# Performance work log

Measured on AMD Instinct MI355X. Metric: run time of the kernel, lower is better.

## Reference

```python
import jax, jax.numpy as jnp
import numpy as np

N = 100000       # nodes
E = 1600000      # edges (before self-loops)
IN = 32          # input_dim
HID = 64         # hidden_dim
HEADS = 4
HO = HID // HEADS  # per-head out of gat1
OUT = 32         # output_dim
HID2 = HID // 2
BN_EPS = 1e-5
NEG_SLOPE = 0.2  # PyG GATConv default leaky relu slope


def setup_inputs() -> dict:
    key = jax.random.key(0)
    ks = jax.random.split(key, 28)
    f32 = jnp.float32
    rn = lambda k, s, sc=0.1: jax.random.normal(k, s, f32) * sc
    inp = {}
    inp["x"] = jax.random.normal(ks[0], (N, IN), f32)
    inp["edge_index"] = jax.random.randint(ks[1], (2, E), 0, N, jnp.int32)
    # GATConv 1: in=IN, heads=HEADS, out/head=HO, concat
    inp["W1"] = rn(ks[2], (IN, HEADS * HO))
    inp["att_src1"] = rn(ks[3], (HEADS, HO))
    inp["att_dst1"] = rn(ks[4], (HEADS, HO))
    inp["b1"] = rn(ks[5], (HEADS * HO,))
    # GATConv 2: in=HID, heads=1, out=OUT, no concat (mean)
    inp["W2"] = rn(ks[6], (HID, OUT))
    inp["att_src2"] = rn(ks[7], (1, OUT))
    inp["att_dst2"] = rn(ks[8], (1, OUT))
    inp["b2"] = rn(ks[9], (OUT,))
    # BatchNorms (inference mode: running stats)
    inp["bn1_g"] = jnp.ones((HID,), f32)
    inp["bn1_b"] = jnp.zeros((HID,), f32)
    inp["bn1_m"] = rn(ks[10], (HID,), 0.1)
    inp["bn1_v"] = jax.random.uniform(ks[11], (HID,), f32, 0.5, 1.5)
    inp["bn2_g"] = jnp.ones((OUT,), f32)
    inp["bn2_b"] = jnp.zeros((OUT,), f32)
    inp["bn2_m"] = rn(ks[12], (OUT,), 0.1)
    inp["bn2_v"] = jax.random.uniform(ks[13], (OUT,), f32, 0.5, 1.5)
    # classifier: OUT -> HID2 -> 3
    inp["cls_w1"] = rn(ks[14], (OUT, HID2))
    inp["cls_b1"] = rn(ks[15], (HID2,))
    inp["cls_w2"] = rn(ks[16], (HID2, 3))
    inp["cls_b2"] = rn(ks[17], (3,))
    inp["reg_w1"] = rn(ks[18], (OUT, HID2))
    inp["reg_b1"] = rn(ks[19], (HID2,))
    inp["reg_w2"] = rn(ks[20], (HID2, 1))
    inp["reg_b2"] = rn(ks[21], (1,))
    return inp


def _segment_softmax(e, seg, n):
    # e: [E, H]; softmax over edges sharing the same destination segment
    m = jax.ops.segment_max(e, seg, num_segments=n)
    ex = jnp.exp(e - m[seg])
    s = jax.ops.segment_sum(ex, seg, num_segments=n)
    return ex / (s[seg] + 1e-16)


def _gat(x, src, dst, W, a_src, a_dst, b, heads, ho, concat):
    n = x.shape[0]
    h = (x @ W).reshape(n, heads, ho)                    # [N,H,F]
    e = (h * a_src).sum(-1)[src] + (h * a_dst).sum(-1)[dst]  # [E,H]
    e = jax.nn.leaky_relu(e, NEG_SLOPE)
    alpha = _segment_softmax(e, dst, n)                  # [E,H]
    out = jax.ops.segment_sum(h[src] * alpha[:, :, None], dst, num_segments=n)
    out = out.reshape(n, heads * ho) if concat else out.mean(axis=1)
    return out + b


def _bn(x, g, b, m, v):
    return (x - m) * jax.lax.rsqrt(v + BN_EPS) * g + b


def reference(x, edge_index, W1, att_src1, att_dst1, b1, W2, att_src2, att_dst2, b2,
              bn1_g, bn1_b, bn1_m, bn1_v, bn2_g, bn2_b, bn2_m, bn2_v,
              cls_w1, cls_b1, cls_w2, cls_b2, reg_w1, reg_b1, reg_w2, reg_b2):
    n = x.shape[0]
    # PyG GATConv default add_self_loops=True
    loops = jnp.arange(n, dtype=edge_index.dtype)
    src = jnp.concatenate([edge_index[0], loops])
    dst = jnp.concatenate([edge_index[1], loops])

    h = _gat(x, src, dst, W1, att_src1, att_dst1, b1, HEADS, HO, True)   # [N, HID]
    h = jax.nn.relu(_bn(h, bn1_g, bn1_b, bn1_m, bn1_v))
    emb = _gat(h, src, dst, W2, att_src2, att_dst2, b2, 1, OUT, False)   # [N, OUT]
    emb = jax.nn.relu(_bn(emb, bn2_g, bn2_b, bn2_m, bn2_v))

    roles = jax.nn.relu(emb @ cls_w1 + cls_b1) @ cls_w2 + cls_b2          # [N, 3]
    energy = jax.nn.relu(emb @ reg_w1 + reg_b1) @ reg_w2 + reg_b2         # [N, 1]
    return emb, roles, energy
```

## Files before the change

kernel.cpp:

```cpp
#include <hip/hip_runtime.h>
#include <hip/hip_bf16.h>

#define NN 100000
#define EE 1600000
#define ETOT (EE + NN)
#define IND 32
#define HIDD 64
#define NHEADS 4
#define OUTD 32
#define HID2D 32

#define BSH 9
#define NBUCK 196
#define CAP 10240
#define EPB 2048

typedef unsigned int uint;

__device__ __forceinline__ uint pack2(float a, float b) {
  uint lo = (uint)__bfloat16_as_ushort(__float2bfloat16(a));
  uint hi = (uint)__bfloat16_as_ushort(__float2bfloat16(b));
  return (hi << 16) | lo;
}
__device__ __forceinline__ float lo2f(uint w) { return __uint_as_float(w << 16); }
__device__ __forceinline__ float hi2f(uint w) { return __uint_as_float(w & 0xFFFF0000u); }

__global__ __launch_bounds__(256) void k_lin1(
    const float* __restrict__ x, const float* __restrict__ W1,
    const float* __restrict__ atsrc, const float* __restrict__ atdst,
    uint* __restrict__ h1u, float* __restrict__ as1, float* __restrict__ ad1) {
  __shared__ float Ws[IND * HIDD];
  __shared__ float xs[8 * IND];
  __shared__ float atS[HIDD], atD[HIDD];
  int t = threadIdx.x;
  for (int i = t; i < IND * HIDD; i += 256) Ws[i] = W1[i];
  if (t < HIDD) { atS[t] = atsrc[t]; atD[t] = atdst[t]; }
  xs[t] = x[blockIdx.x * 256 + t];
  __syncthreads();
  int nl = t >> 5, tl = t & 31;
  int node = blockIdx.x * 8 + nl;
  int j0 = 2 * tl, j1 = j0 + 1;
  float a0 = 0.f, a1 = 0.f;
#pragma unroll
  for (int k = 0; k < IND; k++) {
    float xv = xs[nl * IND + k];
    a0 += xv * Ws[k * HIDD + j0];
    a1 += xv * Ws[k * HIDD + j1];
  }
  h1u[node * 32 + tl] = pack2(a0, a1);
  float ps = a0 * atS[j0] + a1 * atS[j1];
  float pd = a0 * atD[j0] + a1 * atD[j1];
#pragma unroll
  for (int off = 4; off >= 1; off >>= 1) {
    ps += __shfl_down(ps, off, 8);
    pd += __shfl_down(pd, off, 8);
  }
  if ((tl & 7) == 0) {
    as1[node * NHEADS + (tl >> 3)] = ps;
    ad1[node * NHEADS + (tl >> 3)] = pd;
  }
}

__global__ __launch_bounds__(256) void k_lin2(
    const float* __restrict__ hbn, const float* __restrict__ W2,
    const float* __restrict__ atsrc, const float* __restrict__ atdst,
    uint* __restrict__ h2u, float* __restrict__ as2, float* __restrict__ ad2) {
  __shared__ float Ws[HIDD * OUTD];
  __shared__ float xs[16 * HIDD];
  __shared__ float atS[OUTD], atD[OUTD];
  int t = threadIdx.x;
  for (int i = t; i < HIDD * OUTD; i += 256) Ws[i] = W2[i];
  if (t < OUTD) { atS[t] = atsrc[t]; atD[t] = atdst[t]; }
  for (int i = t; i < 16 * HIDD; i += 256) xs[i] = hbn[blockIdx.x * 16 * HIDD + i];
  __syncthreads();
  int nl = t >> 4, tl = t & 15;
  int node = blockIdx.x * 16 + nl;
  int j0 = 2 * tl, j1 = j0 + 1;
  float a0 = 0.f, a1 = 0.f;
#pragma unroll
  for (int k = 0; k < HIDD; k++) {
    float xv = xs[nl * HIDD + k];
    a0 += xv * Ws[k * OUTD + j0];
    a1 += xv * Ws[k * OUTD + j1];
  }
  h2u[node * 16 + tl] = pack2(a0, a1);
  float ps = a0 * atS[j0] + a1 * atS[j1];
  float pd = a0 * atD[j0] + a1 * atD[j1];
#pragma unroll
  for (int off = 8; off >= 1; off >>= 1) {
    ps += __shfl_down(ps, off, 16);
    pd += __shfl_down(pd, off, 16);
  }
  if (tl == 0) { as2[node] = ps; ad2[node] = pd; }
}

__global__ __launch_bounds__(256) void k_bin(const int* __restrict__ ei,
                                             int* __restrict__ bcur,
                                             int* __restrict__ bins) {
  __shared__ int cnt[NBUCK];
  int t = threadIdx.x;
  for (int i = t; i < NBUCK; i += 256) cnt[i] = 0;
  __syncthreads();
  int base = blockIdx.x * EPB;
  int recs[8], bks[8];
#pragma unroll
  for (int k = 0; k < 8; k++) {
    int i = base + k * 256 + t;
    recs[k] = -1; bks[k] = 0;
    if (i < ETOT) {
      int s, d;
      if (i < EE) { s = ei[i]; d = ei[EE + i]; } else { s = i - EE; d = s; }
      recs[k] = (s << BSH) | (d & ((1 << BSH) - 1));
      bks[k] = d >> BSH;
      atomicAdd(&cnt[bks[k]], 1);
    }
  }
  __syncthreads();
  for (int i = t; i < NBUCK; i += 256) cnt[i] = atomicAdd(&bcur[i], cnt[i]);
  __syncthreads();
#pragma unroll
  for (int k = 0; k < 8; k++) {
    if (recs[k] >= 0) {
      int pos = atomicAdd(&cnt[bks[k]], 1);
      bins[bks[k] * CAP + pos] = recs[k];
    }
  }
}

__global__ __launch_bounds__(256) void k_scanb(const int* __restrict__ bcur,
                                               int* __restrict__ gbase,
                                               int* __restrict__ rowp) {
  __shared__ int sA[256], sB[256];
  int t = threadIdx.x;
  int v = (t < NBUCK) ? bcur[t] : 0;
  sA[t] = v;
  __syncthreads();
  int* in = sA; int* out = sB;
  for (int off = 1; off < 256; off <<= 1) {
    out[t] = in[t] + ((t >= off) ? in[t - off] : 0);
    __syncthreads();
    int* tmp = in; in = out; out = tmp;
  }
  if (t < NBUCK) gbase[t] = in[t] - v;
  if (t == 0) rowp[NN] = ETOT;
}

__global__ __launch_bounds__(256) void k_csr(const int* __restrict__ bcur,
                                             const int* __restrict__ gbase,
                                             const int* __restrict__ bins,
                                             int* __restrict__ rowp,
                                             int* __restrict__ srcs) {
  __shared__ int lrec[CAP];
  __shared__ int ldeg[512], sA[512], sB[512];
  int b = blockIdx.x, t = threadIdx.x;
  int count = bcur[b]; if (count > CAP) count = CAP;
  int gb = gbase[b];
  for (int i = t; i < 512; i += 256) ldeg[i] = 0;
  __syncthreads();
  for (int i = t; i < count; i += 256) {
    int r = bins[b * CAP + i];
    lrec[i] = r;
    atomicAdd(&ldeg[r & 511], 1);
  }
  __syncthreads();
  for (int i = t; i < 512; i += 256) sA[i] = ldeg[i];
  __syncthreads();
  int* in = sA; int* out = sB;
  for (int off = 1; off < 512; off <<= 1) {
    for (int i = t; i < 512; i += 256)
      out[i] = in[i] + ((i >= off) ? in[i - off] : 0);
    __syncthreads();
    int* tmp = in; in = out; out = tmp;
  }
  int nb = b << BSH;
  for (int i = t; i < 512; i += 256) {
    int ex = in[i] - ldeg[i];
    if (nb + i < NN) rowp[nb + i] = gb + ex;
    ldeg[i] = ex;
  }
  __syncthreads();
  for (int i = t; i < count; i += 256) {
    int r = lrec[i];
    int pos = atomicAdd(&ldeg[r & 511], 1);
    srcs[gb + pos] = r >> BSH;
  }
}

__global__ __launch_bounds__(256) void k_agg1(
    const int* __restrict__ rowp, const int* __restrict__ srcs,
    const uint* __restrict__ h1u, const float* __restrict__ as1,
    const float* __restrict__ ad1, const float* __restrict__ b1,
    const float* __restrict__ g, const float* __restrict__ bb,
    const float* __restrict__ m, const float* __restrict__ v,
    float* __restrict__ hbn) {
  int t = threadIdx.x;
  int wid = t >> 6, lane = t & 63;
  int node = blockIdx.x * 4 + wid;
  int slot = lane >> 3;
  int fl = lane & 7;
  int hd = fl >> 1;
  int start = rowp[node], end = rowp[node + 1];
  int lastp = end - 1;
  float adv = ad1[node * NHEADS + hd];
  const uint4* h14 = (const uint4*)h1u;
  float acc[8] = {0.f, 0.f, 0.f, 0.f, 0.f, 0.f, 0.f, 0.f};
  float l = 0.f;
  int p = start + slot;
  int pc = p < lastp ? p : lastp;
  int s0 = srcs[pc];
  uint4 w = h14[s0 * 8 + fl];
  float as = as1[s0 * NHEADS + hd];
  int p1 = p + 8;
  int pc1 = p1 < lastp ? p1 : lastp;
  int s1 = srcs[pc1];
  while (p < end) {
    uint4 wn = h14[s1 * 8 + fl];
    float asn = as1[s1 * NHEADS + hd];
    int p2 = p1 + 8;
    int pc2 = p2 < lastp ? p2 : lastp;
    int s2 = srcs[pc2];
    float e = as + adv;
    e = fmaxf(e, 0.2f * e);
    float ex = __expf(e);
    l += ex;
    acc[0] += ex * lo2f(w.x); acc[1] += ex * hi2f(w.x);
    acc[2] += ex * lo2f(w.y); acc[3] += ex * hi2f(w.y);
    acc[4] += ex * lo2f(w.z); acc[5] += ex * hi2f(w.z);
    acc[6] += ex * lo2f(w.w); acc[7] += ex * hi2f(w.w);
    w = wn; as = asn; s1 = s2; p = p1; p1 = p2;
  }
#pragma unroll
  for (int off = 8; off <= 32; off <<= 1) {
#pragma unroll
    for (int i = 0; i < 8; i++) acc[i] += __shfl_xor(acc[i], off, 64);
    l += __shfl_xor(l, off, 64);
  }
  if (slot == 0) {
    float li = 1.f / (l + 1e-16f);
    int fb = fl * 8;
    float o[8];
#pragma unroll
    for (int i = 0; i < 8; i++) {
      int j = fb + i;
      float ov = acc[i] * li + b1[j];
      ov = (ov - m[j]) * rsqrtf(v[j] + 1e-5f) * g[j] + bb[j];
      o[i] = fmaxf(ov, 0.f);
    }
    float4* dst = (float4*)(hbn + node * HIDD + fb);
    dst[0] = make_float4(o[0], o[1], o[2], o[3]);
    dst[1] = make_float4(o[4], o[5], o[6], o[7]);
  }
}

__global__ __launch_bounds__(256) void k_agg2(
    const int* __restrict__ rowp, const int* __restrict__ srcs,
    const uint* __restrict__ h2u, const float* __restrict__ as2,
    const float* __restrict__ ad2, const float* __restrict__ b2v,
    const float* __restrict__ g, const float* __restrict__ bb,
    const float* __restrict__ m, const float* __restrict__ v,
    float* __restrict__ out_emb) {
  int t = threadIdx.x;
  int wid = t >> 6, lane = t & 63;
  int node = blockIdx.x * 4 + wid;
  int slot = lane >> 3;
  int fl = lane & 7;
  int start = rowp[node], end = rowp[node + 1];
  int lastp = end - 1;
  float adv = ad2[node];
  const uint2* h22 = (const uint2*)h2u;
  float acc[4] = {0.f, 0.f, 0.f, 0.f};
  float l = 0.f;
  int p = start + slot;
  int pc = p < lastp ? p : lastp;
  int s0 = srcs[pc];
  uint2 w = h22[s0 * 8 + fl];
  float as = as2[s0];
  int p1 = p + 8;
  int pc1 = p1 < lastp ? p1 : lastp;
  int s1 = srcs[pc1];
  while (p < end) {
    uint2 wn = h22[s1 * 8 + fl];
    float asn = as2[s1];
    int p2 = p1 + 8;
    int pc2 = p2 < lastp ? p2 : lastp;
    int s2 = srcs[pc2];
    float e = as + adv;
    e = fmaxf(e, 0.2f * e);
    float ex = __expf(e);
    l += ex;
    acc[0] += ex * lo2f(w.x); acc[1] += ex * hi2f(w.x);
    acc[2] += ex * lo2f(w.y); acc[3] += ex * hi2f(w.y);
    w = wn; as = asn; s1 = s2; p = p1; p1 = p2;
  }
#pragma unroll
  for (int off = 8; off <= 32; off <<= 1) {
#pragma unroll
    for (int i = 0; i < 4; i++) acc[i] += __shfl_xor(acc[i], off, 64);
    l += __shfl_xor(l, off, 64);
  }
  if (slot == 0) {
    float li = 1.f / (l + 1e-16f);
    int fb = fl * 4;
    float o[4];
#pragma unroll
    for (int i = 0; i < 4; i++) {
      int j = fb + i;
      float ov = acc[i] * li + b2v[j];
      ov = (ov - m[j]) * rsqrtf(v[j] + 1e-5f) * g[j] + bb[j];
      o[i] = fmaxf(ov, 0.f);
    }
    *(float4*)(out_emb + node * OUTD + fb) = make_float4(o[0], o[1], o[2], o[3]);
  }
}

__global__ __launch_bounds__(256) void k_mlp(
    const float* __restrict__ embf,
    const float* __restrict__ cw1, const float* __restrict__ cb1,
    const float* __restrict__ cw2, const float* __restrict__ cb2,
    const float* __restrict__ rw1, const float* __restrict__ rb1,
    const float* __restrict__ rw2, const float* __restrict__ rb2,
    float* __restrict__ out_roles, float* __restrict__ out_energy) {
  __shared__ float C1[OUTD * HID2D], R1[OUTD * HID2D];
  __shared__ float C2[HID2D * 3], CB1[HID2D], RB1[HID2D], R2[HID2D];
  __shared__ float CB2v[3], RB2v;
  int t = threadIdx.x;
  for (int i = t; i < OUTD * HID2D; i += 256) { C1[i] = cw1[i]; R1[i] = rw1[i]; }
  if (t < HID2D) { CB1[t] = cb1[t]; RB1[t] = rb1[t]; R2[t] = rw2[t]; }
  if (t < HID2D * 3) C2[t] = cw2[t];
  if (t < 3) CB2v[t] = cb2[t];
  if (t == 0) RB2v = rb2[0];
  __syncthreads();
  int node = blockIdx.x * 256 + t;
  if (node >= NN) return;
  float e[OUTD];
#pragma unroll
  for (int k = 0; k < OUTD; k++) e[k] = embf[node * OUTD + k];
  float r0 = CB2v[0], r1 = CB2v[1], r2 = CB2v[2], en = RB2v;
  for (int j = 0; j < HID2D; j++) {
    float hc = CB1[j], hr = RB1[j];
#pragma unroll
    for (int k = 0; k < OUTD; k++) {
      hc += e[k] * C1[k * HID2D + j];
      hr += e[k] * R1[k * HID2D + j];
    }
    hc = fmaxf(hc, 0.f);
    hr = fmaxf(hr, 0.f);
    r0 += hc * C2[j * 3 + 0];
    r1 += hc * C2[j * 3 + 1];
    r2 += hc * C2[j * 3 + 2];
    en += hr * R2[j];
  }
  out_roles[node * 3 + 0] = r0;
  out_roles[node * 3 + 1] = r1;
  out_roles[node * 3 + 2] = r2;
  out_energy[node] = en;
}

extern "C" void kernel_launch(void* const* d_in, const int* in_sizes, int n_in,
                              void* d_out, int out_size, void* d_ws, size_t ws_size,
                              hipStream_t stream) {
  const float* x    = (const float*)d_in[0];
  const int*   ei   = (const int*)d_in[1];
  const float* W1   = (const float*)d_in[2];
  const float* as1w = (const float*)d_in[3];
  const float* ad1w = (const float*)d_in[4];
  const float* b1   = (const float*)d_in[5];
  const float* W2   = (const float*)d_in[6];
  const float* as2w = (const float*)d_in[7];
  const float* ad2w = (const float*)d_in[8];
  const float* b2v  = (const float*)d_in[9];
  const float* bn1g = (const float*)d_in[10];
  const float* bn1b = (const float*)d_in[11];
  const float* bn1m = (const float*)d_in[12];
  const float* bn1v = (const float*)d_in[13];
  const float* bn2g = (const float*)d_in[14];
  const float* bn2b = (const float*)d_in[15];
  const float* bn2m = (const float*)d_in[16];
  const float* bn2v = (const float*)d_in[17];
  const float* cw1  = (const float*)d_in[18];
  const float* cb1  = (const float*)d_in[19];
  const float* cw2  = (const float*)d_in[20];
  const float* cb2  = (const float*)d_in[21];
  const float* rw1  = (const float*)d_in[22];
  const float* rb1  = (const float*)d_in[23];
  const float* rw2  = (const float*)d_in[24];
  const float* rb2  = (const float*)d_in[25];

  uint*  h1u = (uint*)d_ws;
  float* hbn = (float*)(h1u + NN * 32);
  float* as1 = hbn + NN * HIDD;
  float* ad1 = as1 + NN * NHEADS;
  int* rowp  = (int*)(ad1 + NN * NHEADS);
  int* srcs  = rowp + NN + 1;
  int* bcur  = srcs + ETOT;
  int* gbase = bcur + 256;
  int* bins  = (int*)hbn;
  uint* h2u  = h1u;
  float* as2 = as1;
  float* ad2 = ad1;

  float* out        = (float*)d_out;
  float* out_emb    = out;
  float* out_roles  = out + NN * OUTD;
  float* out_energy = out + NN * (OUTD + 3);

  hipMemsetAsync(bcur, 0, NBUCK * sizeof(int), stream);
  k_bin<<<(ETOT + EPB - 1) / EPB, 256, 0, stream>>>(ei, bcur, bins);
  k_scanb<<<1, 256, 0, stream>>>(bcur, gbase, rowp);
  k_csr<<<NBUCK, 256, 0, stream>>>(bcur, gbase, bins, rowp, srcs);
  k_lin1<<<NN / 8, 256, 0, stream>>>(x, W1, as1w, ad1w, h1u, as1, ad1);
  k_agg1<<<NN / 4, 256, 0, stream>>>(rowp, srcs, h1u, as1, ad1, b1, bn1g, bn1b, bn1m, bn1v, hbn);
  k_lin2<<<NN / 16, 256, 0, stream>>>(hbn, W2, as2w, ad2w, h2u, as2, ad2);
  k_agg2<<<NN / 4, 256, 0, stream>>>(rowp, srcs, h2u, as2, ad2, b2v, bn2g, bn2b, bn2m, bn2v, out_emb);
  k_mlp<<<(NN + 255) / 256, 256, 0, stream>>>(out_emb, cw1, cb1, cw2, cb2, rw1, rb1, rw2, rb2, out_roles, out_energy);
}
```

Baseline: 359.9 us.

## Fuse lin2 into agg1, MLP heads into agg2, and bucket scan into CSR

Three kernels are folded into their neighbours. The second linear layer and its attention projections now run inside the layer-1 aggregation, using a per-wave row held in shared memory. The classifier and regressor heads now run inside the layer-2 aggregation. The single-block bucket scan is recomputed redundantly in every CSR block. This removes the full-size hbn intermediate and its global round trip, the re-read of the embedding, and three launches. In exchange, every 4-node block reloads the W2 and MLP weights into shared memory, and extra block-wide syncs are added.

Result: slower. 377.3 us (+4.8%).

```diff
diff --git a/kernel.cpp b/kernel.cpp
--- a/kernel.cpp
+++ b/kernel.cpp
@@ -61,39 +61,6 @@
   }
 }
 
-__global__ __launch_bounds__(256) void k_lin2(
-    const float* __restrict__ hbn, const float* __restrict__ W2,
-    const float* __restrict__ atsrc, const float* __restrict__ atdst,
-    uint* __restrict__ h2u, float* __restrict__ as2, float* __restrict__ ad2) {
-  __shared__ float Ws[HIDD * OUTD];
-  __shared__ float xs[16 * HIDD];
-  __shared__ float atS[OUTD], atD[OUTD];
-  int t = threadIdx.x;
-  for (int i = t; i < HIDD * OUTD; i += 256) Ws[i] = W2[i];
-  if (t < OUTD) { atS[t] = atsrc[t]; atD[t] = atdst[t]; }
-  for (int i = t; i < 16 * HIDD; i += 256) xs[i] = hbn[blockIdx.x * 16 * HIDD + i];
-  __syncthreads();
-  int nl = t >> 4, tl = t & 15;
-  int node = blockIdx.x * 16 + nl;
-  int j0 = 2 * tl, j1 = j0 + 1;
-  float a0 = 0.f, a1 = 0.f;
-#pragma unroll
-  for (int k = 0; k < HIDD; k++) {
-    float xv = xs[nl * HIDD + k];
-    a0 += xv * Ws[k * OUTD + j0];
-    a1 += xv * Ws[k * OUTD + j1];
-  }
-  h2u[node * 16 + tl] = pack2(a0, a1);
-  float ps = a0 * atS[j0] + a1 * atS[j1];
-  float pd = a0 * atD[j0] + a1 * atD[j1];
-#pragma unroll
-  for (int off = 8; off >= 1; off >>= 1) {
-    ps += __shfl_down(ps, off, 16);
-    pd += __shfl_down(pd, off, 16);
-  }
-  if (tl == 0) { as2[node] = ps; ad2[node] = pd; }
-}
-
 __global__ __launch_bounds__(256) void k_bin(const int* __restrict__ ei,
                                              int* __restrict__ bcur,
                                              int* __restrict__ bins) {
@@ -127,34 +94,30 @@
   }
 }
 
-__global__ __launch_bounds__(256) void k_scanb(const int* __restrict__ bcur,
-                                               int* __restrict__ gbase,
-                                               int* __restrict__ rowp) {
-  __shared__ int sA[256], sB[256];
-  int t = threadIdx.x;
-  int v = (t < NBUCK) ? bcur[t] : 0;
-  sA[t] = v;
-  __syncthreads();
-  int* in = sA; int* out = sB;
-  for (int off = 1; off < 256; off <<= 1) {
-    out[t] = in[t] + ((t >= off) ? in[t - off] : 0);
-    __syncthreads();
-    int* tmp = in; in = out; out = tmp;
-  }
-  if (t < NBUCK) gbase[t] = in[t] - v;
-  if (t == 0) rowp[NN] = ETOT;
-}
-
 __global__ __launch_bounds__(256) void k_csr(const int* __restrict__ bcur,
-                                             const int* __restrict__ gbase,
                                              const int* __restrict__ bins,
                                              int* __restrict__ rowp,
                                              int* __restrict__ srcs) {
   __shared__ int lrec[CAP];
   __shared__ int ldeg[512], sA[512], sB[512];
   int b = blockIdx.x, t = threadIdx.x;
+  {
+    int v = (t < NBUCK) ? bcur[t] : 0;
+    sA[t] = v;
+    if (t >= 256) sA[t] = 0;
+  }
+  __syncthreads();
+  int* in = sA; int* out = sB;
+  for (int off = 1; off < 256; off <<= 1) {
+    out[t] = in[t] + ((t >= off && t < 256) ? in[t - off] : 0);
+    if (t >= 256) out[t] = 0;
+    __syncthreads();
+    int* tmp = in; in = out; out = tmp;
+  }
+  int gb = (b == 0) ? 0 : in[b - 1];
+  if (b == 0 && t == 0) rowp[NN] = ETOT;
+  __syncthreads();
   int count = bcur[b]; if (count > CAP) count = CAP;
-  int gb = gbase[b];
   for (int i = t; i < 512; i += 256) ldeg[i] = 0;
   __syncthreads();
   for (int i = t; i < count; i += 256) {
@@ -165,7 +128,7 @@
   __syncthreads();
   for (int i = t; i < 512; i += 256) sA[i] = ldeg[i];
   __syncthreads();
-  int* in = sA; int* out = sB;
+  in = sA; out = sB;
   for (int off = 1; off < 512; off <<= 1) {
     for (int i = t; i < 512; i += 256)
       out[i] = in[i] + ((i >= off) ? in[i - off] : 0);
@@ -186,14 +149,22 @@
   }
 }
 
-__global__ __launch_bounds__(256) void k_agg1(
+__global__ __launch_bounds__(256) void k_agg1f(
     const int* __restrict__ rowp, const int* __restrict__ srcs,
     const uint* __restrict__ h1u, const float* __restrict__ as1,
     const float* __restrict__ ad1, const float* __restrict__ b1,
     const float* __restrict__ g, const float* __restrict__ bb,
     const float* __restrict__ m, const float* __restrict__ v,
-    float* __restrict__ hbn) {
+    const float* __restrict__ W2, const float* __restrict__ atsrc2,
+    const float* __restrict__ atdst2,
+    uint* __restrict__ h2u, float* __restrict__ as2, float* __restrict__ ad2) {
+  __shared__ float W2s[HIDD * OUTD];
+  __shared__ float atS2s[OUTD], atD2s[OUTD];
+  __shared__ float rowS[4][HIDD];
   int t = threadIdx.x;
+  for (int i = t; i < HIDD * OUTD; i += 256) W2s[i] = W2[i];
+  if (t < OUTD) { atS2s[t] = atsrc2[t]; atD2s[t] = atdst2[t]; }
+  __syncthreads();
   int wid = t >> 6, lane = t & 63;
   int node = blockIdx.x * 4 + wid;
   int slot = lane >> 3;
@@ -238,28 +209,57 @@
   if (slot == 0) {
     float li = 1.f / (l + 1e-16f);
     int fb = fl * 8;
-    float o[8];
 #pragma unroll
     for (int i = 0; i < 8; i++) {
       int j = fb + i;
       float ov = acc[i] * li + b1[j];
       ov = (ov - m[j]) * rsqrtf(v[j] + 1e-5f) * g[j] + bb[j];
-      o[i] = fmaxf(ov, 0.f);
+      rowS[wid][j] = fmaxf(ov, 0.f);
     }
-    float4* dst = (float4*)(hbn + node * HIDD + fb);
-    dst[0] = make_float4(o[0], o[1], o[2], o[3]);
-    dst[1] = make_float4(o[4], o[5], o[6], o[7]);
-  }
-}
-
-__global__ __launch_bounds__(256) void k_agg2(
+  }
+  __syncthreads();
+  int j = lane & 31, half = lane >> 5;
+  float hv = 0.f;
+#pragma unroll
+  for (int k2 = 0; k2 < 32; k2++) {
+    int k = half * 32 + k2;
+    hv += rowS[wid][k] * W2s[k * OUTD + j];
+  }
+  hv += __shfl_xor(hv, 32, 64);
+  float ps = hv * atS2s[j], pd = hv * atD2s[j];
+#pragma unroll
+  for (int off = 1; off <= 16; off <<= 1) {
+    ps += __shfl_xor(ps, off, 64);
+    pd += __shfl_xor(pd, off, 64);
+  }
+  if (lane == 0) { as2[node] = ps; ad2[node] = pd; }
+  float hn = __shfl_down(hv, 1, 64);
+  if (half == 0 && (j & 1) == 0) h2u[node * 16 + (j >> 1)] = pack2(hv, hn);
+}
+
+__global__ __launch_bounds__(256) void k_agg2f(
     const int* __restrict__ rowp, const int* __restrict__ srcs,
     const uint* __restrict__ h2u, const float* __restrict__ as2,
     const float* __restrict__ ad2, const float* __restrict__ b2v,
     const float* __restrict__ g, const float* __restrict__ bb,
     const float* __restrict__ m, const float* __restrict__ v,
-    float* __restrict__ out_emb) {
+    const float* __restrict__ cw1, const float* __restrict__ cb1,
+    const float* __restrict__ cw2, const float* __restrict__ cb2,
+    const float* __restrict__ rw1, const float* __restrict__ rb1,
+    const float* __restrict__ rw2, const float* __restrict__ rb2,
+    float* __restrict__ out_emb, float* __restrict__ out_roles,
+    float* __restrict__ out_energy) {
+  __shared__ float C1s[OUTD * HID2D], R1s[OUTD * HID2D];
+  __shared__ float C2s[HID2D * 3], R2s[HID2D], CB1s[HID2D], RB1s[HID2D];
+  __shared__ float cb2s[3], rb2s[1];
+  __shared__ float rowE[4][OUTD];
   int t = threadIdx.x;
+  for (int i = t; i < OUTD * HID2D; i += 256) { C1s[i] = cw1[i]; R1s[i] = rw1[i]; }
+  if (t < HID2D) { CB1s[t] = cb1[t]; RB1s[t] = rb1[t]; R2s[t] = rw2[t]; }
+  if (t < HID2D * 3) C2s[t] = cw2[t];
+  if (t < 3) cb2s[t] = cb2[t];
+  if (t == 0) rb2s[0] = rb2[0];
+  __syncthreads();
   int wid = t >> 6, lane = t & 63;
   int node = blockIdx.x * 4 + wid;
   int slot = lane >> 3;
@@ -308,52 +308,38 @@
       float ov = acc[i] * li + b2v[j];
       ov = (ov - m[j]) * rsqrtf(v[j] + 1e-5f) * g[j] + bb[j];
       o[i] = fmaxf(ov, 0.f);
+      rowE[wid][j] = o[i];
     }
     *(float4*)(out_emb + node * OUTD + fb) = make_float4(o[0], o[1], o[2], o[3]);
   }
-}
-
-__global__ __launch_bounds__(256) void k_mlp(
-    const float* __restrict__ embf,
-    const float* __restrict__ cw1, const float* __restrict__ cb1,
-    const float* __restrict__ cw2, const float* __restrict__ cb2,
-    const float* __restrict__ rw1, const float* __restrict__ rb1,
-    const float* __restrict__ rw2, const float* __restrict__ rb2,
-    float* __restrict__ out_roles, float* __restrict__ out_energy) {
-  __shared__ float C1[OUTD * HID2D], R1[OUTD * HID2D];
-  __shared__ float C2[HID2D * 3], CB1[HID2D], RB1[HID2D], R2[HID2D];
-  __shared__ float CB2v[3], RB2v;
-  int t = threadIdx.x;
-  for (int i = t; i < OUTD * HID2D; i += 256) { C1[i] = cw1[i]; R1[i] = rw1[i]; }
-  if (t < HID2D) { CB1[t] = cb1[t]; RB1[t] = rb1[t]; R2[t] = rw2[t]; }
-  if (t < HID2D * 3) C2[t] = cw2[t];
-  if (t < 3) CB2v[t] = cb2[t];
-  if (t == 0) RB2v = rb2[0];
-  __syncthreads();
-  int node = blockIdx.x * 256 + t;
-  if (node >= NN) return;
-  float e[OUTD];
-#pragma unroll
-  for (int k = 0; k < OUTD; k++) e[k] = embf[node * OUTD + k];
-  float r0 = CB2v[0], r1 = CB2v[1], r2 = CB2v[2], en = RB2v;
-  for (int j = 0; j < HID2D; j++) {
-    float hc = CB1[j], hr = RB1[j];
-#pragma unroll
-    for (int k = 0; k < OUTD; k++) {
-      hc += e[k] * C1[k * HID2D + j];
-      hr += e[k] * R1[k * HID2D + j];
-    }
-    hc = fmaxf(hc, 0.f);
-    hr = fmaxf(hr, 0.f);
-    r0 += hc * C2[j * 3 + 0];
-    r1 += hc * C2[j * 3 + 1];
-    r2 += hc * C2[j * 3 + 2];
-    en += hr * R2[j];
-  }
-  out_roles[node * 3 + 0] = r0;
-  out_roles[node * 3 + 1] = r1;
-  out_roles[node * 3 + 2] = r2;
-  out_energy[node] = en;
+  __syncthreads();
+  int j = lane & 31, half = lane >> 5;
+  float a2 = half ? RB1s[j] : CB1s[j];
+  const float* Wm = half ? R1s : C1s;
+#pragma unroll
+  for (int k = 0; k < OUTD; k++) a2 += rowE[wid][k] * Wm[k * HID2D + j];
+  a2 = fmaxf(a2, 0.f);
+  float p0, p1v, p2v;
+  if (half == 0) {
+    p0 = a2 * C2s[j * 3 + 0];
+    p1v = a2 * C2s[j * 3 + 1];
+    p2v = a2 * C2s[j * 3 + 2];
+  } else {
+    p0 = a2 * R2s[j];
+    p1v = 0.f; p2v = 0.f;
+  }
+#pragma unroll
+  for (int off = 1; off <= 16; off <<= 1) {
+    p0 += __shfl_xor(p0, off, 64);
+    p1v += __shfl_xor(p1v, off, 64);
+    p2v += __shfl_xor(p2v, off, 64);
+  }
+  if (lane == 0) {
+    out_roles[node * 3 + 0] = p0 + cb2s[0];
+    out_roles[node * 3 + 1] = p1v + cb2s[1];
+    out_roles[node * 3 + 2] = p2v + cb2s[2];
+  }
+  if (lane == 32) out_energy[node] = p0 + rb2s[0];
 }
 
 extern "C" void kernel_launch(void* const* d_in, const int* in_sizes, int n_in,
@@ -387,17 +373,15 @@
   const float* rb2  = (const float*)d_in[25];
 
   uint*  h1u = (uint*)d_ws;
-  float* hbn = (float*)(h1u + NN * 32);
-  float* as1 = hbn + NN * HIDD;
+  uint*  h2u = h1u + NN * 32;
+  float* as1 = (float*)(h2u + NN * 16);
   float* ad1 = as1 + NN * NHEADS;
-  int* rowp  = (int*)(ad1 + NN * NHEADS);
+  float* as2 = ad1 + NN * NHEADS;
+  float* ad2 = as2 + NN;
+  int* rowp  = (int*)(ad2 + NN);
   int* srcs  = rowp + NN + 1;
   int* bcur  = srcs + ETOT;
-  int* gbase = bcur + 256;
-  int* bins  = (int*)hbn;
-  uint* h2u  = h1u;
-  float* as2 = as1;
-  float* ad2 = ad1;
+  int* bins  = bcur + 256;
 
   float* out        = (float*)d_out;
   float* out_emb    = out;
@@ -406,11 +390,13 @@
 
   hipMemsetAsync(bcur, 0, NBUCK * sizeof(int), stream);
   k_bin<<<(ETOT + EPB - 1) / EPB, 256, 0, stream>>>(ei, bcur, bins);
-  k_scanb<<<1, 256, 0, stream>>>(bcur, gbase, rowp);
-  k_csr<<<NBUCK, 256, 0, stream>>>(bcur, gbase, bins, rowp, srcs);
+  k_csr<<<NBUCK, 256, 0, stream>>>(bcur, bins, rowp, srcs);
   k_lin1<<<NN / 8, 256, 0, stream>>>(x, W1, as1w, ad1w, h1u, as1, ad1);
-  k_agg1<<<NN / 4, 256, 0, stream>>>(rowp, srcs, h1u, as1, ad1, b1, bn1g, bn1b, bn1m, bn1v, hbn);
-  k_lin2<<<NN / 16, 256, 0, stream>>>(hbn, W2, as2w, ad2w, h2u, as2, ad2);
-  k_agg2<<<NN / 4, 256, 0, stream>>>(rowp, srcs, h2u, as2, ad2, b2v, bn2g, bn2b, bn2m, bn2v, out_emb);
-  k_mlp<<<(NN + 255) / 256, 256, 0, stream>>>(out_emb, cw1, cb1, cw2, cb2, rw1, rb1, rw2, rb2, out_roles, out_energy);
-}
+  k_agg1f<<<NN / 4, 256, 0, stream>>>(rowp, srcs, h1u, as1, ad1, b1,
+                                      bn1g, bn1b, bn1m, bn1v,
+                                      W2, as2w, ad2w, h2u, as2, ad2);
+  k_agg2f<<<NN / 4, 256, 0, stream>>>(rowp, srcs, h2u, as2, ad2, b2v,
+                                      bn2g, bn2b, bn2m, bn2v,
+                                      cw1, cb1, cw2, cb2, rw1, rb1, rw2, rb2,
+                                      out_emb, out_roles, out_energy);
+}
```

## Fold bucket scan into CSR kernel and process two nodes per wave in agg1

Applied to the files above, without the earlier changes.

Removes the separate single-block bucket scan launch: each k_csr block now recomputes the 196-entry prefix scan locally to get its base offset. k_agg1 now handles two destination nodes per wavefront with interleaved gathers, raising memory-level parallelism and halving the grid. The bins scratch buffer moves from the hbn region to just after bcur. The trade-off is redundant scan work in every block, plus extra registers and divergent iterations when the two nodes' degrees differ.

After: 346.5 us. 3.7% less time.

```diff
diff --git a/kernel.cpp b/kernel.cpp
--- a/kernel.cpp
+++ b/kernel.cpp
@@ -127,34 +127,25 @@
   }
 }
 
-__global__ __launch_bounds__(256) void k_scanb(const int* __restrict__ bcur,
-                                               int* __restrict__ gbase,
-                                               int* __restrict__ rowp) {
-  __shared__ int sA[256], sB[256];
-  int t = threadIdx.x;
-  int v = (t < NBUCK) ? bcur[t] : 0;
-  sA[t] = v;
-  __syncthreads();
-  int* in = sA; int* out = sB;
-  for (int off = 1; off < 256; off <<= 1) {
-    out[t] = in[t] + ((t >= off) ? in[t - off] : 0);
-    __syncthreads();
-    int* tmp = in; in = out; out = tmp;
-  }
-  if (t < NBUCK) gbase[t] = in[t] - v;
-  if (t == 0) rowp[NN] = ETOT;
-}
-
 __global__ __launch_bounds__(256) void k_csr(const int* __restrict__ bcur,
-                                             const int* __restrict__ gbase,
                                              const int* __restrict__ bins,
                                              int* __restrict__ rowp,
                                              int* __restrict__ srcs) {
   __shared__ int lrec[CAP];
   __shared__ int ldeg[512], sA[512], sB[512];
   int b = blockIdx.x, t = threadIdx.x;
+  sA[t] = (t < NBUCK) ? bcur[t] : 0;
+  __syncthreads();
+  int* in = sA; int* out = sB;
+  for (int off = 1; off < 256; off <<= 1) {
+    out[t] = in[t] + ((t >= off) ? in[t - off] : 0);
+    __syncthreads();
+    int* tmp = in; in = out; out = tmp;
+  }
+  int gb = (b == 0) ? 0 : in[b - 1];
+  if (b == 0 && t == 0) rowp[NN] = ETOT;
+  __syncthreads();
   int count = bcur[b]; if (count > CAP) count = CAP;
-  int gb = gbase[b];
   for (int i = t; i < 512; i += 256) ldeg[i] = 0;
   __syncthreads();
   for (int i = t; i < count; i += 256) {
@@ -165,7 +156,7 @@
   __syncthreads();
   for (int i = t; i < 512; i += 256) sA[i] = ldeg[i];
   __syncthreads();
-  int* in = sA; int* out = sB;
+  in = sA; out = sB;
   for (int off = 1; off < 512; off <<= 1) {
     for (int i = t; i < 512; i += 256)
       out[i] = in[i] + ((i >= off) ? in[i - off] : 0);
@@ -195,54 +186,82 @@
     float* __restrict__ hbn) {
   int t = threadIdx.x;
   int wid = t >> 6, lane = t & 63;
-  int node = blockIdx.x * 4 + wid;
+  int nA = blockIdx.x * 8 + wid * 2;
+  int nB = nA + 1;
   int slot = lane >> 3;
   int fl = lane & 7;
   int hd = fl >> 1;
-  int start = rowp[node], end = rowp[node + 1];
-  int lastp = end - 1;
-  float adv = ad1[node * NHEADS + hd];
+  int stA = rowp[nA], eA = rowp[nA + 1], eB = rowp[nB + 1];
+  int stB = eA;
+  int lpA = eA - 1, lpB = eB - 1;
+  float advA = ad1[nA * NHEADS + hd];
+  float advB = ad1[nB * NHEADS + hd];
   const uint4* h14 = (const uint4*)h1u;
-  float acc[8] = {0.f, 0.f, 0.f, 0.f, 0.f, 0.f, 0.f, 0.f};
-  float l = 0.f;
-  int p = start + slot;
-  int pc = p < lastp ? p : lastp;
-  int s0 = srcs[pc];
-  uint4 w = h14[s0 * 8 + fl];
-  float as = as1[s0 * NHEADS + hd];
-  int p1 = p + 8;
-  int pc1 = p1 < lastp ? p1 : lastp;
-  int s1 = srcs[pc1];
-  while (p < end) {
-    uint4 wn = h14[s1 * 8 + fl];
-    float asn = as1[s1 * NHEADS + hd];
-    int p2 = p1 + 8;
-    int pc2 = p2 < lastp ? p2 : lastp;
-    int s2 = srcs[pc2];
-    float e = as + adv;
-    e = fmaxf(e, 0.2f * e);
-    float ex = __expf(e);
-    l += ex;
-    acc[0] += ex * lo2f(w.x); acc[1] += ex * hi2f(w.x);
-    acc[2] += ex * lo2f(w.y); acc[3] += ex * hi2f(w.y);
-    acc[4] += ex * lo2f(w.z); acc[5] += ex * hi2f(w.z);
-    acc[6] += ex * lo2f(w.w); acc[7] += ex * hi2f(w.w);
-    w = wn; as = asn; s1 = s2; p = p1; p1 = p2;
+  float accA[8] = {0,0,0,0,0,0,0,0}, accB[8] = {0,0,0,0,0,0,0,0};
+  float lA = 0.f, lB = 0.f;
+  int pA = stA + slot, pB = stB + slot;
+  int sA0 = srcs[pA < lpA ? pA : lpA];
+  int sB0 = srcs[pB < lpB ? pB : lpB];
+  uint4 wA = h14[sA0 * 8 + fl];
+  uint4 wB = h14[sB0 * 8 + fl];
+  float asA = as1[sA0 * NHEADS + hd];
+  float asB = as1[sB0 * NHEADS + hd];
+  int p1A = pA + 8, p1B = pB + 8;
+  int sA1 = srcs[p1A < lpA ? p1A : lpA];
+  int sB1 = srcs[p1B < lpB ? p1B : lpB];
+  while (pA < eA || pB < eB) {
+    uint4 wnA = h14[sA1 * 8 + fl];
+    uint4 wnB = h14[sB1 * 8 + fl];
+    float anA = as1[sA1 * NHEADS + hd];
+    float anB = as1[sB1 * NHEADS + hd];
+    int p2A = p1A + 8, p2B = p1B + 8;
+    int sA2 = srcs[p2A < lpA ? p2A : lpA];
+    int sB2 = srcs[p2B < lpB ? p2B : lpB];
+    if (pA < eA) {
+      float e = asA + advA;
+      e = fmaxf(e, 0.2f * e);
+      float ex = __expf(e);
+      lA += ex;
+      accA[0] += ex * lo2f(wA.x); accA[1] += ex * hi2f(wA.x);
+      accA[2] += ex * lo2f(wA.y); accA[3] += ex * hi2f(wA.y);
+      accA[4] += ex * lo2f(wA.z); accA[5] += ex * hi2f(wA.z);
+      accA[6] += ex * lo2f(wA.w); accA[7] += ex * hi2f(wA.w);
+    }
+    if (pB < eB) {
+      float e = asB + advB;
+      e = fmaxf(e, 0.2f * e);
+      float ex = __expf(e);
+      lB += ex;
+      accB[0] += ex * lo2f(wB.x); accB[1] += ex * hi2f(wB.x);
+      accB[2] += ex * lo2f(wB.y); accB[3] += ex * hi2f(wB.y);
+      accB[4] += ex * lo2f(wB.z); accB[5] += ex * hi2f(wB.z);
+      accB[6] += ex * lo2f(wB.w); accB[7] += ex * hi2f(wB.w);
+    }
+    wA = wnA; wB = wnB; asA = anA; asB = anB;
+    sA1 = sA2; sB1 = sB2;
+    pA = p1A; pB = p1B; p1A = p2A; p1B = p2B;
   }
 #pragma unroll
   for (int off = 8; off <= 32; off <<= 1) {
 #pragma unroll
-    for (int i = 0; i < 8; i++) acc[i] += __shfl_xor(acc[i], off, 64);
-    l += __shfl_xor(l, off, 64);
-  }
-  if (slot == 0) {
-    float li = 1.f / (l + 1e-16f);
+    for (int i = 0; i < 8; i++) {
+      accA[i] += __shfl_xor(accA[i], off, 64);
+      accB[i] += __shfl_xor(accB[i], off, 64);
+    }
+    lA += __shfl_xor(lA, off, 64);
+    lB += __shfl_xor(lB, off, 64);
+  }
+  if (slot < 2) {
+    int node = slot == 0 ? nA : nB;
+    float lsum = slot == 0 ? lA : lB;
+    float li = 1.f / (lsum + 1e-16f);
     int fb = fl * 8;
     float o[8];
 #pragma unroll
     for (int i = 0; i < 8; i++) {
       int j = fb + i;
-      float ov = acc[i] * li + b1[j];
+      float av = slot == 0 ? accA[i] : accB[i];
+      float ov = av * li + b1[j];
       ov = (ov - m[j]) * rsqrtf(v[j] + 1e-5f) * g[j] + bb[j];
       o[i] = fmaxf(ov, 0.f);
     }
@@ -393,8 +412,7 @@
   int* rowp  = (int*)(ad1 + NN * NHEADS);
   int* srcs  = rowp + NN + 1;
   int* bcur  = srcs + ETOT;
-  int* gbase = bcur + 256;
-  int* bins  = (int*)hbn;
+  int* bins  = bcur + 256;
   uint* h2u  = h1u;
   float* as2 = as1;
   float* ad2 = ad1;
@@ -406,10 +424,9 @@
 
   hipMemsetAsync(bcur, 0, NBUCK * sizeof(int), stream);
   k_bin<<<(ETOT + EPB - 1) / EPB, 256, 0, stream>>>(ei, bcur, bins);
-  k_scanb<<<1, 256, 0, stream>>>(bcur, gbase, rowp);
-  k_csr<<<NBUCK, 256, 0, stream>>>(bcur, gbase, bins, rowp, srcs);
+  k_csr<<<NBUCK, 256, 0, stream>>>(bcur, bins, rowp, srcs);
   k_lin1<<<NN / 8, 256, 0, stream>>>(x, W1, as1w, ad1w, h1u, as1, ad1);
-  k_agg1<<<NN / 4, 256, 0, stream>>>(rowp, srcs, h1u, as1, ad1, b1, bn1g, bn1b, bn1m, bn1v, hbn);
+  k_agg1<<<NN / 8, 256, 0, stream>>>(rowp, srcs, h1u, as1, ad1, b1, bn1g, bn1b, bn1m, bn1v, hbn);
   k_lin2<<<NN / 16, 256, 0, stream>>>(hbn, W2, as2w, ad2w, h2u, as2, ad2);
   k_agg2<<<NN / 4, 256, 0, stream>>>(rowp, srcs, h2u, as2, ad2, b2v, bn2g, bn2b, bn2m, bn2v, out_emb);
   k_mlp<<<(NN + 255) / 256, 256, 0, stream>>>(out_emb, cw1, cb1, cw2, cb2, rw1, rb1, rw2, rb2, out_roles, out_energy);
```
